# Optimization experiments

Measured on AMD Instinct MI355X. Metric: run time of the kernel, lower is better.

## Reference

```python
import jax, jax.numpy as jnp
import numpy as np

B, T, E = 4, 2048, 512
H, D = 8, 64            # num_heads, head_size = E // H
HID = H * E             # FFN hidden = num_heads * n_embed (per source)
EPS = 1e-5


def layer_norm(x, g, b):
    mu = jnp.mean(x, axis=-1, keepdims=True)
    var = jnp.var(x, axis=-1, keepdims=True)
    return (x - mu) * jax.lax.rsqrt(var + EPS) * g + b


def setup_inputs() -> dict:
    key = jax.random.key(0)
    ks = jax.random.split(key, 12)
    s_e = 1.0 / np.sqrt(E)
    s_hd = 1.0 / np.sqrt(H * D)
    s_hid = 1.0 / np.sqrt(HID)
    return {
        "x": jax.random.normal(ks[0], (B, T, E), jnp.float32),
        "Wq": jax.random.normal(ks[1], (H, E, D), jnp.float32) * s_e,
        "Wk": jax.random.normal(ks[2], (H, E, D), jnp.float32) * s_e,
        "Wv": jax.random.normal(ks[3], (H, E, D), jnp.float32) * s_e,
        "Wo": jax.random.normal(ks[4], (H * D, E), jnp.float32) * s_hd,
        "bo": jnp.zeros((E,), jnp.float32),
        "W1": jax.random.normal(ks[5], (E, HID), jnp.float32) * s_e,
        "b1": jnp.zeros((HID,), jnp.float32),
        "W2": jax.random.normal(ks[6], (HID, E), jnp.float32) * s_hid,
        "b2": jnp.zeros((E,), jnp.float32),
        "g1": jnp.ones((E,), jnp.float32),
        "be1": jnp.zeros((E,), jnp.float32),
        "g2": jnp.ones((E,), jnp.float32),
        "be2": jnp.zeros((E,), jnp.float32),
    }


def reference(x, Wq, Wk, Wv, Wo, bo, W1, b1, W2, b2, g1, be1, g2, be2):
    # pre-LN decoder block (layer_norm_first=True path)
    xn = layer_norm(x, g1, be1)

    # multi-head causal attention; NOTE: scale is T**-0.5 per the source code
    q = jnp.einsum('bte,hed->bhtd', xn, Wq)
    k = jnp.einsum('bte,hed->bhtd', xn, Wk)
    v = jnp.einsum('bte,hed->bhtd', xn, Wv)
    scores = jnp.einsum('bhtd,bhsd->bhts', q, k) * (T ** -0.5)
    causal = jnp.tril(jnp.ones((T, T), bool))
    scores = jnp.where(causal, scores, -jnp.inf)
    attn = jax.nn.softmax(scores, axis=-1)
    o = jnp.einsum('bhts,bhsd->bhtd', attn, v)           # [B,H,T,D]
    o = o.transpose(0, 2, 1, 3).reshape(B, T, H * D)      # concat heads
    mha = o @ Wo + bo

    x = xn + mha
    xn2 = layer_norm(x, g2, be2)
    ffn = jax.nn.relu(xn2 @ W1 + b1) @ W2 + b2
    return xn2 + ffn
```

## Files before the change

kernel.cpp:

```cpp
#include <hip/hip_runtime.h>
#include <hip/hip_bf16.h>
#include <math.h>

#define Bsz 4
#define Tt 2048
#define Ee 512
#define Hh 8
#define Dd 64
#define HIDs 4096
#define Mrows (Bsz * Tt)

typedef __attribute__((ext_vector_type(8))) short short8;
typedef __attribute__((ext_vector_type(4))) float f32x4;
typedef __attribute__((ext_vector_type(16))) float f32x16;

#define AS1 __attribute__((address_space(1)))
#define AS3 __attribute__((address_space(3)))

__device__ __forceinline__ unsigned short f2bfu(float f) {
    unsigned u = __float_as_uint(f);
    return (unsigned short)((u + 0x7fffu + ((u >> 16) & 1u)) >> 16);
}
__device__ __forceinline__ unsigned short truncbf(float f) {
    return (unsigned short)(__float_as_uint(f) >> 16);
}

__device__ __forceinline__ short8 ld_sw(const __hip_bfloat16* base, int R, int sl) {
    return *(const short8*)(base + R * 32 + (((sl) ^ ((R >> 1) & 3)) << 3));
}

__device__ __forceinline__ void ln_body(const float* __restrict__ x,
        const float* __restrict__ g, const float* __restrict__ b,
        const float* __restrict__ addb,
        float* __restrict__ out_f, __hip_bfloat16* __restrict__ out_bf,
        int row) {
    int tid = threadIdx.x;
    const float* xr = x + (size_t)row * Ee;
    float v0 = xr[tid];
    float v1 = xr[tid + 256];
    float s = v0 + v1;
    float sq = v0 * v0 + v1 * v1;
#pragma unroll
    for (int off = 32; off > 0; off >>= 1) {
        s  += __shfl_xor(s, off, 64);
        sq += __shfl_xor(sq, off, 64);
    }
    __shared__ float ls[4], lq[4];
    int wid = tid >> 6, lane = tid & 63;
    if (lane == 0) { ls[wid] = s; lq[wid] = sq; }
    __syncthreads();
    s  = ls[0] + ls[1] + ls[2] + ls[3];
    sq = lq[0] + lq[1] + lq[2] + lq[3];
    float mean = s * (1.0f / Ee);
    float var  = sq * (1.0f / Ee) - mean * mean;
    float rstd = rsqrtf(var + 1e-5f);
    float o0 = (v0 - mean) * rstd * g[tid]       + b[tid];
    float o1 = (v1 - mean) * rstd * g[tid + 256] + b[tid + 256];
    float* orow = out_f + (size_t)row * Ee;
    orow[tid]       = o0 + addb[tid];
    orow[tid + 256] = o1 + addb[tid + 256];
    __hip_bfloat16* brow = out_bf + (size_t)row * Ee;
    brow[tid]       = __float2bfloat16(o0);
    brow[tid + 256] = __float2bfloat16(o1);
}

__global__ __launch_bounds__(256) void ln_kernel(const float* __restrict__ x,
        const float* __restrict__ g, const float* __restrict__ b,
        const float* __restrict__ addb,
        float* __restrict__ out_f, __hip_bfloat16* __restrict__ out_bf) {
    ln_body(x, g, b, addb, out_f, out_bf, blockIdx.x);
}

__device__ __forceinline__ void tr_tile(const float* __restrict__ in,
        __hip_bfloat16* __restrict__ outp, int R, int C, int c0, int r0) {
    __shared__ float tile[64][65];
    int tc = threadIdx.x & 63, tg = threadIdx.x >> 6;
#pragma unroll
    for (int i = 0; i < 16; ++i) {
        int r = tg * 16 + i;
        tile[r][tc] = in[(size_t)(r0 + r) * C + c0 + tc];
    }
    __syncthreads();
#pragma unroll
    for (int i = 0; i < 16; ++i) {
        int cc = tg * 16 + i;
        outp[(size_t)(c0 + cc) * R + r0 + tc] = __float2bfloat16(tile[tc][cc]);
    }
}
__global__ __launch_bounds__(256) void startup_kernel(
        const float* __restrict__ x, const float* __restrict__ g1,
        const float* __restrict__ be1, const float* __restrict__ bo,
        float* __restrict__ xn, __hip_bfloat16* __restrict__ xn_bf,
        const float* __restrict__ Wq, const float* __restrict__ Wk,
        const float* __restrict__ Wv, const float* __restrict__ Wo,
        const float* __restrict__ W1, const float* __restrict__ W2,
        __hip_bfloat16* __restrict__ bqT, __hip_bfloat16* __restrict__ woT,
        __hip_bfloat16* __restrict__ w1T, __hip_bfloat16* __restrict__ w2T) {
    if (blockIdx.x < Mrows) {
        ln_body(x, g1, be1, bo, xn, xn_bf, blockIdx.x);
        return;
    }
    int blk = blockIdx.x - Mrows;
    if (blk < 192) {
        int p = blk >> 6, h = (blk >> 3) & 7, et = blk & 7;
        const float* W = (p == 0) ? Wq : ((p == 1) ? Wk : Wv);
        float sc = (p == 0) ? 0.022097086912079608f * 1.4426950408889634f : 1.0f;
        __shared__ float tile[64][65];
        int td = threadIdx.x & 63, tg = threadIdx.x >> 6;
#pragma unroll
        for (int i = 0; i < 16; ++i) {
            int e = tg * 16 + i;
            tile[e][td] = W[((size_t)h * Ee + et * 64 + e) * Dd + td] * sc;
        }
        __syncthreads();
#pragma unroll
        for (int i = 0; i < 16; ++i) {
            int d = tg * 16 + i;
            bqT[((size_t)(p * 512 + h * 64 + d)) * Ee + et * 64 + td] =
                __float2bfloat16(tile[td][d]);
        }
    } else if (blk < 256) {
        int t = blk - 192;
        tr_tile(Wo, woT, 512, 512, (t & 7) * 64, (t >> 3) * 64);
    } else if (blk < 768) {
        int t = blk - 256;
        tr_tile(W1, w1T, 512, HIDs, (t & 63) * 64, (t >> 6) * 64);
    } else {
        int t = blk - 768;
        tr_tile(W2, w2T, HIDs, 512, (t & 7) * 64, (t >> 3) * 64);
    }
}

__global__ __launch_bounds__(256) void mfma_gemm(
        const __hip_bfloat16* __restrict__ A, int lda,
        const __hip_bfloat16* __restrict__ B, int ldb,
        __hip_bfloat16* __restrict__ Cb, int ldc, int K, int nx) {
    __shared__ __hip_bfloat16 S[32768];
    int tid = threadIdx.x;
    int lane = tid & 63, wave = tid >> 6;
    int wm = wave >> 1, wn = wave & 1;
    int L = blockIdx.x;
    int slots = (int)gridDim.x >> 3;
    int v = (L & 7) * slots + (L >> 3);
    int bx = v % nx, by = v / nx;
    int row0 = by * 128, col0 = bx * 128;
    f32x4 acc[4][4];
#pragma unroll
    for (int i = 0; i < 4; ++i)
#pragma unroll
        for (int j = 0; j < 4; ++j) acc[i][j] = (f32x4){0.f, 0.f, 0.f, 0.f};

    int fr = lane & 15, sl = lane >> 4;
    int T = K >> 6;

#define STAGEQ(tt, bb)                                                        \
    do {                                                                      \
        int kk_ = (tt) * 64;                                                  \
        _Pragma("unroll")                                                     \
        for (int j = 0; j < 4; ++j) {                                         \
            int c = j * 256 + tid;                                            \
            int p = c >> 9, cp = c & 511;                                     \
            int r = cp >> 2, s = cp & 3;                                      \
            int kg = ((s ^ ((r >> 1) & 3)) << 3);                             \
            int cb = j * 256 + wave * 64;                                     \
            int ko = kk_ + p * 32 + kg;                                       \
            __builtin_amdgcn_global_load_lds(                                 \
                (const AS1 void*)(A + (size_t)(row0 + r) * lda + ko),         \
                (AS3 void*)(S + (bb) * 16384 + cb * 8), 16, 0, 0);            \
            __builtin_amdgcn_global_load_lds(                                 \
                (const AS1 void*)(B + (size_t)(col0 + r) * ldb + ko),         \
                (AS3 void*)(S + (bb) * 16384 + 8192 + cb * 8), 16, 0, 0);     \
        }                                                                     \
    } while (0)

    STAGEQ(0, 0);
    for (int t = 0; t < T; ++t) {
        int tn = (t + 1 < T) ? t + 1 : 0;
        STAGEQ(tn, (t + 1) & 1);
        asm volatile("s_waitcnt vmcnt(8)" ::: "memory");
        __builtin_amdgcn_s_barrier();
        asm volatile("" ::: "memory");
        const __hip_bfloat16* Ab = S + (t & 1) * 16384;
        const __hip_bfloat16* Bb = Ab + 8192;
#pragma unroll
        for (int ks = 0; ks < 2; ++ks) {
            short8 afr[4], bfr[4];
#pragma unroll
            for (int i = 0; i < 4; ++i) {
                afr[i] = ld_sw(Ab + ks * 4096, wm * 64 + i * 16 + fr, sl);
                bfr[i] = ld_sw(Bb + ks * 4096, wn * 64 + i * 16 + fr, sl);
            }
#pragma unroll
            for (int i = 0; i < 4; ++i)
#pragma unroll
                for (int j = 0; j < 4; ++j)
                    acc[i][j] = __builtin_amdgcn_mfma_f32_16x16x32_bf16(afr[i], bfr[j], acc[i][j], 0, 0, 0);
        }
        asm volatile("" ::: "memory");
        __builtin_amdgcn_s_barrier();
        asm volatile("" ::: "memory");
    }
#undef STAGEQ
    asm volatile("s_waitcnt vmcnt(0)" ::: "memory");
    __syncthreads();
    unsigned short* Ew = (unsigned short*)S + wave * 1152;
    const __hip_bfloat16* Er = (const __hip_bfloat16*)Ew;
    int rq = (lane >> 4) << 2;
    int rr = lane >> 2, cb2 = (lane & 3) * 16;
#pragma unroll
    for (int i = 0; i < 4; ++i) {
#pragma unroll
        for (int j = 0; j < 4; ++j)
#pragma unroll
            for (int gi = 0; gi < 4; ++gi)
                Ew[(rq + gi) * 72 + j * 16 + fr] = f2bfu(acc[i][j][gi]);
        uint4 v0 = *(const uint4*)(Er + rr * 72 + cb2);
        uint4 v1 = *(const uint4*)(Er + rr * 72 + cb2 + 8);
        size_t rg = (size_t)(row0 + wm * 64 + i * 16 + rr) * ldc + col0 + wn * 64 + cb2;
        *(uint4*)(Cb + rg)     = v0;
        *(uint4*)(Cb + rg + 8) = v1;
    }
}

__global__ __launch_bounds__(256) void mfma_gemm_sk(
        const __hip_bfloat16* __restrict__ A, int lda,
        const __hip_bfloat16* __restrict__ B, int ldb,
        float* __restrict__ Cf, int ldc, int Ksp, int nx) {
    __shared__ __hip_bfloat16 S[32768];
    int tid = threadIdx.x;
    int lane = tid & 63, wave = tid >> 6;
    int wm = wave >> 1, wn = wave & 1;
    int L = blockIdx.x;
    int slots = (int)gridDim.x >> 3;
    int v = (L & 7) * slots + (L >> 3);
    int kq = v & 1;
    int u = v >> 1;
    int bx = u % nx, by = u / nx;
    int row0 = by * 128, col0 = bx * 128;
    A += (size_t)kq * Ksp;
    B += (size_t)kq * Ksp;
    f32x4 acc[4][4];
#pragma unroll
    for (int i = 0; i < 4; ++i)
#pragma unroll
        for (int j = 0; j < 4; ++j) acc[i][j] = (f32x4){0.f, 0.f, 0.f, 0.f};

    int fr = lane & 15, sl = lane >> 4;
    int T = Ksp >> 6;

#define STAGES(tt, bb)                                                        \
    do {                                                                      \
        int kk_ = (tt) * 64;                                                  \
        _Pragma("unroll")                                                     \
        for (int j = 0; j < 4; ++j) {                                         \
            int c = j * 256 + tid;                                            \
            int p = c >> 9, cp = c & 511;                                     \
            int r = cp >> 2, s = cp & 3;                                      \
            int kg = ((s ^ ((r >> 1) & 3)) << 3);                             \
            int cb = j * 256 + wave * 64;                                     \
            int ko = kk_ + p * 32 + kg;                                       \
            __builtin_amdgcn_global_load_lds(                                 \
                (const AS1 void*)(A + (size_t)(row0 + r) * lda + ko),         \
                (AS3 void*)(S + (bb) * 16384 + cb * 8), 16, 0, 0);            \
            __builtin_amdgcn_global_load_lds(                                 \
                (const AS1 void*)(B + (size_t)(col0 + r) * ldb + ko),         \
                (AS3 void*)(S + (bb) * 16384 + 8192 + cb * 8), 16, 0, 0);     \
        }                                                                     \
    } while (0)

    STAGES(0, 0);
    for (int t = 0; t < T; ++t) {
        int tn = (t + 1 < T) ? t + 1 : 0;
        STAGES(tn, (t + 1) & 1);
        asm volatile("s_waitcnt vmcnt(8)" ::: "memory");
        __builtin_amdgcn_s_barrier();
        asm volatile("" ::: "memory");
        const __hip_bfloat16* Ab = S + (t & 1) * 16384;
        const __hip_bfloat16* Bb = Ab + 8192;
#pragma unroll
        for (int ks = 0; ks < 2; ++ks) {
            short8 afr[4], bfr[4];
#pragma unroll
            for (int i = 0; i < 4; ++i) {
                afr[i] = ld_sw(Ab + ks * 4096, wm * 64 + i * 16 + fr, sl);
                bfr[i] = ld_sw(Bb + ks * 4096, wn * 64 + i * 16 + fr, sl);
            }
#pragma unroll
            for (int i = 0; i < 4; ++i)
#pragma unroll
                for (int j = 0; j < 4; ++j)
                    acc[i][j] = __builtin_amdgcn_mfma_f32_16x16x32_bf16(afr[i], bfr[j], acc[i][j], 0, 0, 0);
        }
        asm volatile("" ::: "memory");
        __builtin_amdgcn_s_barrier();
        asm volatile("" ::: "memory");
    }
#undef STAGES
    asm volatile("s_waitcnt vmcnt(0)" ::: "memory");
    int rq = (lane >> 4) << 2;
#pragma unroll
    for (int i = 0; i < 4; ++i)
#pragma unroll
        for (int j = 0; j < 4; ++j)
#pragma unroll
            for (int gi = 0; gi < 4; ++gi) {
                int r = row0 + wm * 64 + i * 16 + rq + gi;
                int c = col0 + wn * 64 + j * 16 + fr;
                unsafeAtomicAdd(&Cf[(size_t)r * ldc + c], acc[i][j][gi]);
            }
}

__global__ __launch_bounds__(256) void mfma_gemm_n64(
        const __hip_bfloat16* __restrict__ A, int lda,
        const __hip_bfloat16* __restrict__ B, int ldb,
        float* __restrict__ Cf, int ldc, int K, int nx) {
    __shared__ __hip_bfloat16 S[36864];
    int tid = threadIdx.x;
    int lane = tid & 63, wave = tid >> 6;
    int L = blockIdx.x;
    int slots = (int)gridDim.x >> 3;
    int v = (L & 7) * slots + (L >> 3);
    int bx = v % nx, by = v / nx;
    int row0 = by * 128, col0 = bx * 64;
    f32x4 acc[2][4];
#pragma unroll
    for (int i = 0; i < 2; ++i)
#pragma unroll
        for (int j = 0; j < 4; ++j) acc[i][j] = (f32x4){0.f, 0.f, 0.f, 0.f};

    int fr = lane & 15, sl = lane >> 4;
    int T = K >> 6;

#define STAGEN(tt, bb)                                                        \
    do {                                                                      \
        int kk_ = (tt) * 64;                                                  \
        _Pragma("unroll")                                                     \
        for (int j = 0; j < 4; ++j) {                                         \
            int c = j * 256 + tid;                                            \
            int p = c >> 9, cp = c & 511;                                     \
            int r = cp >> 2, s = cp & 3;                                      \
            int kg = ((s ^ ((r >> 1) & 3)) << 3);                             \
            int cb = j * 256 + wave * 64;                                     \
            __builtin_amdgcn_global_load_lds(                                 \
                (const AS1 void*)(A + (size_t)(row0 + r) * lda + kk_ + p * 32 + kg), \
                (AS3 void*)(S + (bb) * 12288 + cb * 8), 16, 0, 0);            \
        }                                                                     \
        _Pragma("unroll")                                                     \
        for (int j = 0; j < 2; ++j) {                                         \
            int c = j * 256 + tid;                                            \
            int p = c >> 8, cp = c & 255;                                     \
            int r = cp >> 2, s = cp & 3;                                      \
            int kg = ((s ^ ((r >> 1) & 3)) << 3);                             \
            int cb = j * 256 + wave * 64;                                     \
            __builtin_amdgcn_global_load_lds(                                 \
                (const AS1 void*)(B + (size_t)(col0 + r) * ldb + kk_ + p * 32 + kg), \
                (AS3 void*)(S + (bb) * 12288 + 8192 + cb * 8), 16, 0, 0);     \
        }                                                                     \
    } while (0)

    STAGEN(0, 0);
    STAGEN(1, 1);
    for (int t = 0; t < T; ++t) {
        int tn = (t + 2 < T) ? t + 2 : 0;
        STAGEN(tn, (t + 2) % 3);
        asm volatile("s_waitcnt vmcnt(12)" ::: "memory");
        __builtin_amdgcn_s_barrier();
        asm volatile("" ::: "memory");
        const __hip_bfloat16* Ab = S + (t % 3) * 12288;
        const __hip_bfloat16* Bb = Ab + 8192;
#pragma unroll
        for (int ks = 0; ks < 2; ++ks) {
            short8 afr[2], bfr[4];
#pragma unroll
            for (int i = 0; i < 2; ++i)
                afr[i] = ld_sw(Ab + ks * 4096, wave * 32 + i * 16 + fr, sl);
#pragma unroll
            for (int j = 0; j < 4; ++j)
                bfr[j] = ld_sw(Bb + ks * 2048, j * 16 + fr, sl);
#pragma unroll
            for (int i = 0; i < 2; ++i)
#pragma unroll
                for (int j = 0; j < 4; ++j)
                    acc[i][j] = __builtin_amdgcn_mfma_f32_16x16x32_bf16(afr[i], bfr[j], acc[i][j], 0, 0, 0);
        }
        asm volatile("" ::: "memory");
        __builtin_amdgcn_s_barrier();
        asm volatile("" ::: "memory");
    }
#undef STAGEN
    asm volatile("s_waitcnt vmcnt(0)" ::: "memory");
    int rq = (lane >> 4) << 2;
#pragma unroll
    for (int i = 0; i < 2; ++i)
#pragma unroll
        for (int j = 0; j < 4; ++j)
#pragma unroll
            for (int gidx = 0; gidx < 4; ++gidx) {
                int r = row0 + wave * 32 + i * 16 + rq + gidx;
                int c = col0 + j * 16 + fr;
                Cf[(size_t)r * ldc + c] += acc[i][j][gidx];
            }
}

__device__ __forceinline__ short8 ld_frag(const __hip_bfloat16* base, int r, int slot) {
    return *(const short8*)(base + r * 64 + ((slot ^ (r & 7)) << 3));
}

__global__ __launch_bounds__(512, 2) void gemm256_8ph(
        const __hip_bfloat16* __restrict__ A, int lda,
        const __hip_bfloat16* __restrict__ B, int ldb,
        __hip_bfloat16* __restrict__ Cb, int ldc, int K,
        const float* __restrict__ bias, int nx) {
    __shared__ __hip_bfloat16 S[65536];
    __hip_bfloat16* Asb = S;
    __hip_bfloat16* Bsb = S + 32768;
    int tid = threadIdx.x;
    int lane = tid & 63, wave = tid >> 6;
    int wm = wave >> 2, wn = wave & 3;
    int fr = lane & 15, l5 = lane >> 4;
    int L = blockIdx.x;
    int slots = (int)gridDim.x >> 3;
    int v = (L & 7) * slots + (L >> 3);
    int bx = v % nx, by = v / nx;
    int row0 = by * 256, col0 = bx * 256;
    int T = K >> 6;

    f32x4 acc[8][4];
#pragma unroll
    for (int i = 0; i < 8; ++i)
#pragma unroll
        for (int j = 0; j < 4; ++j) acc[i][j] = (f32x4){0.f, 0.f, 0.f, 0.f};

#define STAGE_A(tt, hh, bb)                                                   \
    do {                                                                      \
        _Pragma("unroll")                                                     \
        for (int j = 0; j < 2; ++j) {                                         \
            int c = j * 512 + tid;                                            \
            int r = c >> 3;                                                   \
            int sl = (c & 7) ^ (r & 7);                                       \
            int cb = j * 512 + wave * 64;                                     \
            int grow = row0 + ((r >> 6) << 7) + (hh) * 64 + (r & 63);         \
            __builtin_amdgcn_global_load_lds(                                 \
                (const AS1 void*)(A + (size_t)grow * lda + (tt) * 64 + sl * 8), \
                (AS3 void*)(Asb + (bb) * 16384 + (hh) * 8192 + cb * 8), 16, 0, 0); \
        }                                                                     \
    } while (0)
#define STAGE_B(tt, hh, bb)                                                   \
    do {                                                                      \
        _Pragma("unroll")                                                     \
        for (int j = 0; j < 2; ++j) {                                         \
            int c = j * 512 + tid;                                            \
            int r = c >> 3;                                                   \
            int sl = (c & 7) ^ (r & 7);                                       \
            int cb = j * 512 + wave * 64;                                     \
            int gcol = col0 + ((r >> 5) << 6) + (hh) * 32 + (r & 31);         \
            __builtin_amdgcn_global_load_lds(                                 \
                (const AS1 void*)(B + (size_t)gcol * ldb + (tt) * 64 + sl * 8), \
                (AS3 void*)(Bsb + (bb) * 16384 + (hh) * 8192 + cb * 8), 16, 0, 0); \
        }                                                                     \
    } while (0)

    STAGE_A(0, 0, 0);
    STAGE_B(0, 0, 0);
    STAGE_B(0, 1, 0);
    STAGE_A(0, 1, 0);

    short8 a[4][2], b[2][2][2];
    for (int t = 0; t < T; ++t) {
        int buf = t & 1, nb = buf ^ 1;
        int tn = (t + 1 < T) ? t + 1 : 0;
        const __hip_bfloat16* Ab0 = Asb + buf * 16384;
        const __hip_bfloat16* Ab1 = Ab0 + 8192;
        const __hip_bfloat16* Bb0 = Bsb + buf * 16384;
        const __hip_bfloat16* Bb1 = Bb0 + 8192;

        STAGE_A(tn, 0, nb);
        asm volatile("s_waitcnt vmcnt(6)" ::: "memory");
        __builtin_amdgcn_s_barrier();
        asm volatile("" ::: "memory");
#pragma unroll
        for (int i = 0; i < 4; ++i)
#pragma unroll
            for (int ks = 0; ks < 2; ++ks)
                a[i][ks] = ld_frag(Ab0, wm * 64 + i * 16 + fr, ks * 4 + l5);
#pragma unroll
        for (int jj = 0; jj < 2; ++jj)
#pragma unroll
            for (int ks = 0; ks < 2; ++ks)
                b[0][jj][ks] = ld_frag(Bb0, wn * 32 + jj * 16 + fr, ks * 4 + l5);
        __builtin_amdgcn_s_setprio(1);
#pragma unroll
        for (int i = 0; i < 4; ++i)
#pragma unroll
            for (int jj = 0; jj < 2; ++jj)
#pragma unroll
                for (int ks = 0; ks < 2; ++ks)
                    acc[i][jj] = __builtin_amdgcn_mfma_f32_16x16x32_bf16(
                        a[i][ks], b[0][jj][ks], acc[i][jj], 0, 0, 0);
        __builtin_amdgcn_s_setprio(0);
        asm volatile("" ::: "memory");
        __builtin_amdgcn_s_barrier();
        asm volatile("" ::: "memory");

        STAGE_B(tn, 0, nb);
        asm volatile("s_waitcnt vmcnt(6)" ::: "memory");
        __builtin_amdgcn_s_barrier();
        asm volatile("" ::: "memory");
#pragma unroll
        for (int jj = 0; jj < 2; ++jj)
#pragma unroll
            for (int ks = 0; ks < 2; ++ks)
                b[1][jj][ks] = ld_frag(Bb1, wn * 32 + jj * 16 + fr, ks * 4 + l5);
        __builtin_amdgcn_s_setprio(1);
#pragma unroll
        for (int i = 0; i < 4; ++i)
#pragma unroll
            for (int jj = 0; jj < 2; ++jj)
#pragma unroll
                for (int ks = 0; ks < 2; ++ks)
                    acc[i][2 + jj] = __builtin_amdgcn_mfma_f32_16x16x32_bf16(
                        a[i][ks], b[1][jj][ks], acc[i][2 + jj], 0, 0, 0);
        __builtin_amdgcn_s_setprio(0);
        asm volatile("" ::: "memory");
        __builtin_amdgcn_s_barrier();
        asm volatile("" ::: "memory");

        STAGE_B(tn, 1, nb);
        asm volatile("s_waitcnt vmcnt(6)" ::: "memory");
        __builtin_amdgcn_s_barrier();
        asm volatile("" ::: "memory");
#pragma unroll
        for (int i = 0; i < 4; ++i)
#pragma unroll
            for (int ks = 0; ks < 2; ++ks)
                a[i][ks] = ld_frag(Ab1, wm * 64 + i * 16 + fr, ks * 4 + l5);
        __builtin_amdgcn_s_setprio(1);
#pragma unroll
        for (int i = 0; i < 4; ++i)
#pragma unroll
            for (int jj = 0; jj < 2; ++jj)
#pragma unroll
                for (int ks = 0; ks < 2; ++ks)
                    acc[4 + i][2 + jj] = __builtin_amdgcn_mfma_f32_16x16x32_bf16(
                        a[i][ks], b[1][jj][ks], acc[4 + i][2 + jj], 0, 0, 0);
        __builtin_amdgcn_s_setprio(0);
        asm volatile("" ::: "memory");
        __builtin_amdgcn_s_barrier();
        asm volatile("" ::: "memory");

        STAGE_A(tn, 1, nb);
        asm volatile("" ::: "memory");
        __builtin_amdgcn_s_barrier();
        asm volatile("" ::: "memory");
        __builtin_amdgcn_s_setprio(1);
#pragma unroll
        for (int i = 0; i < 4; ++i)
#pragma unroll
            for (int jj = 0; jj < 2; ++jj)
#pragma unroll
                for (int ks = 0; ks < 2; ++ks)
                    acc[4 + i][jj] = __builtin_amdgcn_mfma_f32_16x16x32_bf16(
                        a[i][ks], b[0][jj][ks], acc[4 + i][jj], 0, 0, 0);
        __builtin_amdgcn_s_setprio(0);
        asm volatile("" ::: "memory");
        __builtin_amdgcn_s_barrier();
        asm volatile("" ::: "memory");
    }
#undef STAGE_A
#undef STAGE_B

    __syncthreads();
    float bvv[4];
#pragma unroll
    for (int nj = 0; nj < 4; ++nj) bvv[nj] = bias[col0 + wn * 64 + nj * 16 + fr];
    unsigned short* Ew = (unsigned short*)S + wave * 1152;
    const __hip_bfloat16* Er = (const __hip_bfloat16*)Ew;
    int rq = l5 << 2;
    int rr = lane >> 2, cb2 = (lane & 3) * 16;
#pragma unroll
    for (int mi = 0; mi < 8; ++mi) {
#pragma unroll
        for (int nj = 0; nj < 4; ++nj)
#pragma unroll
            for (int gi = 0; gi < 4; ++gi) {
                float tv = acc[mi][nj][gi] + bvv[nj];
                Ew[(rq + gi) * 72 + nj * 16 + fr] = f2bfu(tv > 0.f ? tv : 0.f);
            }
        uint4 v0 = *(const uint4*)(Er + rr * 72 + cb2);
        uint4 v1 = *(const uint4*)(Er + rr * 72 + cb2 + 8);
        size_t rg = (size_t)(row0 + wm * 128 + mi * 16 + rr) * ldc
                    + col0 + wn * 64 + cb2;
        *(uint4*)(Cb + rg)     = v0;
        *(uint4*)(Cb + rg + 8) = v1;
    }
}

__global__ __launch_bounds__(256) void attn_mfma(const __hip_bfloat16* __restrict__ qkvb,
        __hip_bfloat16* __restrict__ ob) {
    __shared__ __hip_bfloat16 KsS[2][64 * 72];
    __shared__ __hip_bfloat16 VtS[2][64 * 72];
    __shared__ __hip_bfloat16 PsS[4 * 32 * 72];
    __hip_bfloat16* Qs = PsS;

    const unsigned short* q16 = (const unsigned short*)qkvb;
    int tid  = threadIdx.x;
    int lane = tid & 63, wave = tid >> 6;
    int l31 = lane & 31, l5 = lane >> 5;
    int blk = blockIdx.x;
    int qb  = 15 - (blk >> 5);
    int bh  = blk & 31;
    int b = bh >> 3, h = bh & 7;
    int base = qb * 128;
    size_t tokbase = (size_t)b * Tt;
    int qoff = h * 64, koff = 512 + h * 64, voff = 1024 + h * 64;

    {
        int q = tid >> 1, dg = (tid & 1) * 32;
        const unsigned short* src = q16 + (tokbase + base + q) * 1536 + qoff + dg;
        uint4 a  = *(const uint4*)src;
        uint4 b4 = *(const uint4*)(src + 8);
        uint4 c4 = *(const uint4*)(src + 16);
        uint4 d4 = *(const uint4*)(src + 24);
        *(uint4*)(Qs + q * 72 + dg)      = a;
        *(uint4*)(Qs + q * 72 + dg + 8)  = b4;
        *(uint4*)(Qs + q * 72 + dg + 16) = c4;
        *(uint4*)(Qs + q * 72 + dg + 24) = d4;
    }
    __syncthreads();
    short8 aq[4];
#pragma unroll
    for (int kd = 0; kd < 4; ++kd)
        aq[kd] = *(const short8*)(Qs + (wave * 32 + l31) * 72 + kd * 16 + l5 * 8);

    short8 ones;
#pragma unroll
    for (int i = 0; i < 8; ++i) ones[i] = (short)0x3F80;

    f32x16 acc[2], accL;
#pragma unroll
    for (int i = 0; i < 16; ++i) { acc[0][i] = 0.f; acc[1][i] = 0.f; accL[i] = 0.f; }
    __hip_bfloat16* Psw = PsS + wave * (32 * 72);
    unsigned short* Psw16 = (unsigned short*)Psw;

    int s_k = tid >> 2, dg_k = (tid & 3) * 16;
    int sp = (tid & 31) * 2, dg8 = (tid >> 5) * 8;
    uint4 kr0, kr1, va, vb;
    {
        const unsigned short* kp = q16 + (tokbase + s_k) * 1536 + koff + dg_k;
        kr0 = *(const uint4*)kp;
        kr1 = *(const uint4*)(kp + 8);
        const unsigned short* vp = q16 + (tokbase + sp) * 1536 + voff + dg8;
        va = *(const uint4*)vp;
        vb = *(const uint4*)(vp + 1536);
    }

    int tmax = 2 * qb + 1;
    for (int tile = 0; tile <= tmax; ++tile) {
        int buf = tile & 1;
        *(uint4*)(KsS[buf] + s_k * 72 + dg_k)     = kr0;
        *(uint4*)(KsS[buf] + s_k * 72 + dg_k + 8) = kr1;
        {
            unsigned a0[4] = {va.x, va.y, va.z, va.w};
            unsigned b0[4] = {vb.x, vb.y, vb.z, vb.w};
#pragma unroll
            for (int i = 0; i < 4; ++i) {
                unsigned p0 = (a0[i] & 0xffffu) | (b0[i] << 16);
                unsigned p1 = (a0[i] >> 16) | (b0[i] & 0xffff0000u);
                *(unsigned*)(VtS[buf] + (dg8 + 2 * i) * 72 + sp)     = p0;
                *(unsigned*)(VtS[buf] + (dg8 + 2 * i + 1) * 72 + sp) = p1;
            }
        }
        __syncthreads();
        if (tile < tmax) {
            int s1 = (tile + 1) * 64;
            const unsigned short* kp = q16 + (tokbase + s1 + s_k) * 1536 + koff + dg_k;
            kr0 = *(const uint4*)kp;
            kr1 = *(const uint4*)(kp + 8);
            const unsigned short* vp = q16 + (tokbase + s1 + sp) * 1536 + voff + dg8;
            va = *(const uint4*)vp;
            vb = *(const uint4*)(vp + 1536);
        }
        if (tile == tmax && wave < 2) continue;
        f32x16 Sc[2];
#pragma unroll
        for (int i = 0; i < 16; ++i) { Sc[0][i] = 0.f; Sc[1][i] = 0.f; }
#pragma unroll
        for (int st = 0; st < 2; ++st)
#pragma unroll
            for (int kd = 0; kd < 4; ++kd) {
                short8 bk = *(const short8*)(KsS[buf] + (st * 32 + l31) * 72 + kd * 16 + l5 * 8);
                Sc[st] = __builtin_amdgcn_mfma_f32_32x32x16_bf16(aq[kd], bk, Sc[st], 0, 0, 0);
            }
        if (tile >= 2 * qb) {
            int s0t = tile * 64;
            int qrb = base + wave * 32 + 4 * l5;
#pragma unroll
            for (int st = 0; st < 2; ++st) {
                int sg = s0t + st * 32 + l31;
#pragma unroll
                for (int reg = 0; reg < 16; ++reg) {
                    int qr = qrb + (reg & 3) + 8 * (reg >> 2);
                    if (sg > qr) Sc[st][reg] = -1e30f;
                }
            }
        }
#pragma unroll
        for (int st = 0; st < 2; ++st)
#pragma unroll
            for (int reg = 0; reg < 16; ++reg) {
                int pr = (reg & 3) + 8 * (reg >> 2) + 4 * l5;
                Psw16[pr * 72 + st * 32 + l31] =
                    truncbf(__builtin_amdgcn_exp2f(Sc[st][reg]));
            }
#pragma unroll
        for (int ks = 0; ks < 4; ++ks) {
            short8 ap = *(const short8*)(Psw + l31 * 72 + ks * 16 + l5 * 8);
            accL = __builtin_amdgcn_mfma_f32_32x32x16_bf16(ap, ones, accL, 0, 0, 0);
#pragma unroll
            for (int dt = 0; dt < 2; ++dt) {
                short8 bv = *(const short8*)(VtS[buf] + (dt * 32 + l31) * 72 + ks * 16 + l5 * 8);
                acc[dt] = __builtin_amdgcn_mfma_f32_32x32x16_bf16(ap, bv, acc[dt], 0, 0, 0);
            }
        }
    }
#pragma unroll
    for (int reg = 0; reg < 16; ++reg) {
        float rl = 1.0f / accL[reg];
        int qr = base + wave * 32 + (reg & 3) + 8 * (reg >> 2) + 4 * l5;
#pragma unroll
        for (int dt = 0; dt < 2; ++dt)
            ob[(tokbase + qr) * 512 + h * 64 + dt * 32 + l31] =
                __float2bfloat16(acc[dt][reg] * rl);
    }
}

extern "C" void kernel_launch(void* const* d_in, const int* in_sizes, int n_in,
                              void* d_out, int out_size, void* d_ws, size_t ws_size,
                              hipStream_t stream) {
    const float* x   = (const float*)d_in[0];
    const float* Wq  = (const float*)d_in[1];
    const float* Wk  = (const float*)d_in[2];
    const float* Wv  = (const float*)d_in[3];
    const float* Wo  = (const float*)d_in[4];
    const float* bo  = (const float*)d_in[5];
    const float* W1  = (const float*)d_in[6];
    const float* b1  = (const float*)d_in[7];
    const float* W2  = (const float*)d_in[8];
    const float* b2  = (const float*)d_in[9];
    const float* g1  = (const float*)d_in[10];
    const float* be1 = (const float*)d_in[11];
    const float* g2  = (const float*)d_in[12];
    const float* be2 = (const float*)d_in[13];
    float* out = (float*)d_out;

    char* ws = (char*)d_ws;
    __hip_bfloat16* bqT    = (__hip_bfloat16*)(ws);
    __hip_bfloat16* woT    = (__hip_bfloat16*)(ws + 1572864);
    __hip_bfloat16* w1T    = (__hip_bfloat16*)(ws + 2097152);
    __hip_bfloat16* w2T    = (__hip_bfloat16*)(ws + 6291456);
    float*          xn     = (float*)(ws + 10485760);
    __hip_bfloat16* xn_bf  = (__hip_bfloat16*)(ws + 27262976);
    __hip_bfloat16* qkv_bf = (__hip_bfloat16*)(ws + 35651584);
    __hip_bfloat16* o_bf   = (__hip_bfloat16*)(ws + 60817408);
    __hip_bfloat16* h_bf   = (__hip_bfloat16*)(ws + 35651584);

    startup_kernel<<<Mrows + 1280, 256, 0, stream>>>(
        x, g1, be1, bo, xn, xn_bf, Wq, Wk, Wv, Wo, W1, W2, bqT, woT, w1T, w2T);
    mfma_gemm<<<768, 256, 0, stream>>>(
        xn_bf, 512, bqT, 512, qkv_bf, 1536, 512, 12);
    attn_mfma<<<Bsz * Hh * (Tt / 128), 256, 0, stream>>>(qkv_bf, o_bf);
    mfma_gemm_n64<<<512, 256, 0, stream>>>(
        o_bf, 512, woT, 512, xn, 512, 512, 8);
    ln_kernel<<<Mrows, 256, 0, stream>>>(xn, g2, be2, b2, out, xn_bf);
    gemm256_8ph<<<512, 512, 0, stream>>>(
        xn_bf, 512, w1T, 512, h_bf, HIDs, 512, b1, 16);
    mfma_gemm_sk<<<512, 256, 0, stream>>>(
        h_bf, HIDs, w2T, HIDs, out, 512, 2048, 4);
}
```

Baseline: 297.1 us.

## Replace FFN down-projection split-K GEMM with 128x256 tile, triple-buffered kernel

```diff
diff --git a/kernel.cpp b/kernel.cpp
--- a/kernel.cpp
+++ b/kernel.cpp
@@ -220,94 +220,6 @@
         *(uint4*)(Cb + rg)     = v0;
         *(uint4*)(Cb + rg + 8) = v1;
     }
-}
-
-__global__ __launch_bounds__(256) void mfma_gemm_sk(
-        const __hip_bfloat16* __restrict__ A, int lda,
-        const __hip_bfloat16* __restrict__ B, int ldb,
-        float* __restrict__ Cf, int ldc, int Ksp, int nx) {
-    __shared__ __hip_bfloat16 S[32768];
-    int tid = threadIdx.x;
-    int lane = tid & 63, wave = tid >> 6;
-    int wm = wave >> 1, wn = wave & 1;
-    int L = blockIdx.x;
-    int slots = (int)gridDim.x >> 3;
-    int v = (L & 7) * slots + (L >> 3);
-    int kq = v & 1;
-    int u = v >> 1;
-    int bx = u % nx, by = u / nx;
-    int row0 = by * 128, col0 = bx * 128;
-    A += (size_t)kq * Ksp;
-    B += (size_t)kq * Ksp;
-    f32x4 acc[4][4];
-#pragma unroll
-    for (int i = 0; i < 4; ++i)
-#pragma unroll
-        for (int j = 0; j < 4; ++j) acc[i][j] = (f32x4){0.f, 0.f, 0.f, 0.f};
-
-    int fr = lane & 15, sl = lane >> 4;
-    int T = Ksp >> 6;
-
-#define STAGES(tt, bb)                                                        \
-    do {                                                                      \
-        int kk_ = (tt) * 64;                                                  \
-        _Pragma("unroll")                                                     \
-        for (int j = 0; j < 4; ++j) {                                         \
-            int c = j * 256 + tid;                                            \
-            int p = c >> 9, cp = c & 511;                                     \
-            int r = cp >> 2, s = cp & 3;                                      \
-            int kg = ((s ^ ((r >> 1) & 3)) << 3);                             \
-            int cb = j * 256 + wave * 64;                                     \
-            int ko = kk_ + p * 32 + kg;                                       \
-            __builtin_amdgcn_global_load_lds(                                 \
-                (const AS1 void*)(A + (size_t)(row0 + r) * lda + ko),         \
-                (AS3 void*)(S + (bb) * 16384 + cb * 8), 16, 0, 0);            \
-            __builtin_amdgcn_global_load_lds(                                 \
-                (const AS1 void*)(B + (size_t)(col0 + r) * ldb + ko),         \
-                (AS3 void*)(S + (bb) * 16384 + 8192 + cb * 8), 16, 0, 0);     \
-        }                                                                     \
-    } while (0)
-
-    STAGES(0, 0);
-    for (int t = 0; t < T; ++t) {
-        int tn = (t + 1 < T) ? t + 1 : 0;
-        STAGES(tn, (t + 1) & 1);
-        asm volatile("s_waitcnt vmcnt(8)" ::: "memory");
-        __builtin_amdgcn_s_barrier();
-        asm volatile("" ::: "memory");
-        const __hip_bfloat16* Ab = S + (t & 1) * 16384;
-        const __hip_bfloat16* Bb = Ab + 8192;
-#pragma unroll
-        for (int ks = 0; ks < 2; ++ks) {
-            short8 afr[4], bfr[4];
-#pragma unroll
-            for (int i = 0; i < 4; ++i) {
-                afr[i] = ld_sw(Ab + ks * 4096, wm * 64 + i * 16 + fr, sl);
-                bfr[i] = ld_sw(Bb + ks * 4096, wn * 64 + i * 16 + fr, sl);
-            }
-#pragma unroll
-            for (int i = 0; i < 4; ++i)
-#pragma unroll
-                for (int j = 0; j < 4; ++j)
-                    acc[i][j] = __builtin_amdgcn_mfma_f32_16x16x32_bf16(afr[i], bfr[j], acc[i][j], 0, 0, 0);
-        }
-        asm volatile("" ::: "memory");
-        __builtin_amdgcn_s_barrier();
-        asm volatile("" ::: "memory");
-    }
-#undef STAGES
-    asm volatile("s_waitcnt vmcnt(0)" ::: "memory");
-    int rq = (lane >> 4) << 2;
-#pragma unroll
-    for (int i = 0; i < 4; ++i)
-#pragma unroll
-        for (int j = 0; j < 4; ++j)
-#pragma unroll
-            for (int gi = 0; gi < 4; ++gi) {
-                int r = row0 + wm * 64 + i * 16 + rq + gi;
-                int c = col0 + wn * 64 + j * 16 + fr;
-                unsafeAtomicAdd(&Cf[(size_t)r * ldc + c], acc[i][j][gi]);
-            }
 }
 
 __global__ __launch_bounds__(256) void mfma_gemm_n64(
@@ -399,6 +311,103 @@
                 int r = row0 + wave * 32 + i * 16 + rq + gidx;
                 int c = col0 + j * 16 + fr;
                 Cf[(size_t)r * ldc + c] += acc[i][j][gidx];
+            }
+}
+
+__global__ __launch_bounds__(256, 1) void gemm_n256(
+        const __hip_bfloat16* __restrict__ A, int lda,
+        const __hip_bfloat16* __restrict__ B, int ldb,
+        float* __restrict__ Cf, int ldc, int Ksp) {
+    __shared__ __hip_bfloat16 S[3 * 24576];
+    int tid = threadIdx.x;
+    int lane = tid & 63, wave = tid >> 6;
+    int wm = wave >> 1, wn = wave & 1;
+    int L = blockIdx.x;
+    int slots = (int)gridDim.x >> 3;
+    int v = (L & 7) * slots + (L >> 3);
+    int kq = v & 1;
+    int u = v >> 1;
+    int bx = u & 1, by = u >> 1;
+    int row0 = by * 128, col0 = bx * 256;
+    A += (size_t)kq * Ksp;
+    B += (size_t)kq * Ksp;
+    f32x4 acc[4][8];
+#pragma unroll
+    for (int i = 0; i < 4; ++i)
+#pragma unroll
+        for (int j = 0; j < 8; ++j) acc[i][j] = (f32x4){0.f, 0.f, 0.f, 0.f};
+
+    int fr = lane & 15, sl = lane >> 4;
+    int T = Ksp >> 6;
+
+#define STG256(tt, bb)                                                        \
+    do {                                                                      \
+        int kk_ = (tt) * 64;                                                  \
+        _Pragma("unroll")                                                     \
+        for (int j = 0; j < 4; ++j) {                                         \
+            int c = j * 256 + tid;                                            \
+            int p = c >> 9, cp = c & 511;                                     \
+            int r = cp >> 2, s = cp & 3;                                      \
+            int kg = ((s ^ ((r >> 1) & 3)) << 3);                             \
+            int cb = j * 256 + wave * 64;                                     \
+            __builtin_amdgcn_global_load_lds(                                 \
+                (const AS1 void*)(A + (size_t)(row0 + r) * lda + kk_ + p * 32 + kg), \
+                (AS3 void*)(S + (bb) * 24576 + cb * 8), 16, 0, 0);            \
+        }                                                                     \
+        _Pragma("unroll")                                                     \
+        for (int j = 0; j < 8; ++j) {                                         \
+            int c = j * 256 + tid;                                            \
+            int p = c >> 10, cp = c & 1023;                                   \
+            int r = cp >> 2, s = cp & 3;                                      \
+            int kg = ((s ^ ((r >> 1) & 3)) << 3);                             \
+            int cb = j * 256 + wave * 64;                                     \
+            __builtin_amdgcn_global_load_lds(                                 \
+                (const AS1 void*)(B + (size_t)(col0 + r) * ldb + kk_ + p * 32 + kg), \
+                (AS3 void*)(S + (bb) * 24576 + 8192 + cb * 8), 16, 0, 0);     \
+        }                                                                     \
+    } while (0)
+
+    STG256(0, 0);
+    STG256(1, 1);
+    for (int t = 0; t < T; ++t) {
+        int tn = (t + 2 < T) ? t + 2 : 0;
+        STG256(tn, (t + 2) % 3);
+        asm volatile("s_waitcnt vmcnt(24)" ::: "memory");
+        __builtin_amdgcn_s_barrier();
+        asm volatile("" ::: "memory");
+        const __hip_bfloat16* Ab = S + (t % 3) * 24576;
+        const __hip_bfloat16* Bb = Ab + 8192;
+#pragma unroll
+        for (int ks = 0; ks < 2; ++ks) {
+            short8 afr[4], bfr[8];
+#pragma unroll
+            for (int i = 0; i < 4; ++i)
+                afr[i] = ld_sw(Ab + ks * 4096, wm * 64 + i * 16 + fr, sl);
+#pragma unroll
+            for (int j = 0; j < 8; ++j)
+                bfr[j] = ld_sw(Bb + ks * 8192, wn * 128 + j * 16 + fr, sl);
+#pragma unroll
+            for (int i = 0; i < 4; ++i)
+#pragma unroll
+                for (int j = 0; j < 8; ++j)
+                    acc[i][j] = __builtin_amdgcn_mfma_f32_16x16x32_bf16(afr[i], bfr[j], acc[i][j], 0, 0, 0);
+        }
+        asm volatile("" ::: "memory");
+        __builtin_amdgcn_s_barrier();
+        asm volatile("" ::: "memory");
+    }
+#undef STG256
+    asm volatile("s_waitcnt vmcnt(0)" ::: "memory");
+    int rq = (lane >> 4) << 2;
+#pragma unroll
+    for (int i = 0; i < 4; ++i)
+#pragma unroll
+        for (int j = 0; j < 8; ++j)
+#pragma unroll
+            for (int gi = 0; gi < 4; ++gi) {
+                int r = row0 + wm * 64 + i * 16 + rq + gi;
+                int c = col0 + wn * 128 + j * 16 + fr;
+                unsafeAtomicAdd(&Cf[(size_t)r * ldc + c], acc[i][j][gi]);
             }
 }
 
@@ -774,6 +783,6 @@
     ln_kernel<<<Mrows, 256, 0, stream>>>(xn, g2, be2, b2, out, xn_bf);
     gemm256_8ph<<<512, 512, 0, stream>>>(
         xn_bf, 512, w1T, 512, h_bf, HIDs, 512, b1, 16);
-    mfma_gemm_sk<<<512, 256, 0, stream>>>(
-        h_bf, HIDs, w2T, HIDs, out, 512, 2048, 4);
-}
+    gemm_n256<<<256, 256, 0, stream>>>(
+        h_bf, HIDs, w2T, HIDs, out, 512, 2048);
+}
```

Measured after the change: 325.9 us. 1.1x slower.
